# Kernel tuning notes

Hardware: AMD Instinct MI355X
Metric: run time of the kernel (lower is better)

## Reference

```python
import jax, jax.numpy as jnp
import numpy as np

B, L, HID = 2, 2048, 4096
NH, NKV, HD = 16, 4, 64
BLOCK = 16
THETA = 8000000.0
EPS = 1e-6
NEG = jnp.finfo(jnp.float32).min


def _rope_tables(theta, L, hd):
    inv_freq = 1.0 / (theta ** (np.arange(0, hd, 2, dtype=np.float32) / hd))  # [hd/2]
    t = np.arange(L, dtype=np.float32)
    freqs = np.outer(t, inv_freq)                      # [L, hd/2]
    emb = np.concatenate([freqs, freqs], axis=-1)      # [L, hd]
    return jnp.asarray(np.cos(emb)), jnp.asarray(np.sin(emb))


def setup_inputs() -> dict:
    key = jax.random.key(0)
    k1, k2, k3 = jax.random.split(key, 3)
    hidden_states = jax.random.normal(k1, (B, L, HID), dtype=jnp.float32)
    Wqkv = jax.random.normal(k2, (HID, (NH + 2 * NKV) * HD), dtype=jnp.float32) * 0.006
    Wo = jax.random.normal(k3, (NH * HD, HID), dtype=jnp.float32) * 0.006
    q_norm_w = jnp.ones((HD,), dtype=jnp.float32)
    k_norm_w = jnp.ones((HD,), dtype=jnp.float32)
    # block-diagonal causal additive mask [1,1,L,L]
    idx = jnp.arange(L)
    same_block = (idx[:, None] // BLOCK) == (idx[None, :] // BLOCK)
    causal = idx[:, None] >= idx[None, :]
    attention_mask = jnp.where(same_block & causal, 0.0, NEG)[None, None].astype(jnp.float32)
    cos1, sin1 = _rope_tables(THETA, L, HD)
    cos = jnp.broadcast_to(cos1[None], (B, L, HD))
    sin = jnp.broadcast_to(sin1[None], (B, L, HD))
    return {"hidden_states": hidden_states, "attention_mask": attention_mask,
            "cos": cos, "sin": sin, "Wqkv": Wqkv, "Wo": Wo,
            "q_norm_w": q_norm_w, "k_norm_w": k_norm_w}


def _rms_norm(x, w):
    xf = x.astype(jnp.float32)
    var = jnp.mean(xf * xf, axis=-1, keepdims=True)
    return (xf * jax.lax.rsqrt(var + EPS)).astype(x.dtype) * w


def _rotate_half(x):
    x1, x2 = jnp.split(x, 2, axis=-1)
    return jnp.concatenate([-x2, x1], axis=-1)


def reference(hidden_states, attention_mask, cos, sin, Wqkv, Wo, q_norm_w, k_norm_w):
    Bc, Lc, _ = hidden_states.shape
    qkv = hidden_states @ Wqkv                                # [B,L,(NH+2NKV)*HD]
    qkv = qkv.reshape(Bc, Lc, NH + 2 * NKV, HD)
    q, k, v = jnp.split(qkv, [NH, NH + NKV], axis=2)
    q = q.transpose(0, 2, 1, 3)                               # [B,NH,L,HD]
    k = k.transpose(0, 2, 1, 3)                               # [B,NKV,L,HD]
    v = v.transpose(0, 2, 1, 3)
    q = _rms_norm(q, q_norm_w)
    k = _rms_norm(k, k_norm_w)
    c = cos[:, None]                                          # [B,1,L,HD]
    s = sin[:, None]
    q = q * c + _rotate_half(q) * s
    k = k * c + _rotate_half(k) * s
    groups = NH // NKV
    k = jnp.repeat(k, groups, axis=1)                         # [B,NH,L,HD]
    v = jnp.repeat(v, groups, axis=1)
    scale = 1.0 / jnp.sqrt(jnp.float32(HD))
    scores = jnp.einsum('bhqd,bhkd->bhqk', q, k) * scale + attention_mask
    probs = jax.nn.softmax(scores, axis=-1)
    out = jnp.einsum('bhqk,bhkd->bhqd', probs, v)             # [B,NH,L,HD]
    out = out.transpose(0, 2, 1, 3).reshape(Bc, Lc, NH * HD)
    return out @ Wo
```

## Files before the change

kernel.cpp:

```cpp
#include <hip/hip_runtime.h>
#include <hip/hip_bf16.h>
#include <cstdint>

#define B_SZ   2
#define L_SEQ  2048
#define HID    4096
#define NH     16
#define NKV    4
#define HD     64
#define NQKV   (NH + 2*NKV)
#define QKV_N  (NQKV*HD)
#define O_N    (NH*HD)
#define M_ROWS (B_SZ*L_SEQ)
#define EPSV   1e-6f

typedef __bf16  bf16x8_t  __attribute__((ext_vector_type(8)));
typedef float   f32x4_t   __attribute__((ext_vector_type(4)));
typedef unsigned short ushort8_t __attribute__((ext_vector_type(8)));

__device__ __forceinline__ unsigned short f2b(float f) {
    union { float f; uint32_t u; } v; v.f = f;
    uint32_t r = v.u + 0x7FFFu + ((v.u >> 16) & 1u);
    return (unsigned short)(r >> 16);
}
__device__ __forceinline__ float b2f(unsigned short u) {
    union { uint32_t u; float f; } v; v.u = ((uint32_t)u) << 16;
    return v.f;
}

__device__ __forceinline__ void gload_lds16(const void* g, void* l) {
    __builtin_amdgcn_global_load_lds(
        (__attribute__((address_space(1))) void*)(g),
        (__attribute__((address_space(3))) void*)(l),
        16, 0, 0);
}

#define BARF() do { asm volatile("" ::: "memory"); \
                    __builtin_amdgcn_s_barrier();  \
                    asm volatile("" ::: "memory"); } while (0)

template <int N> __device__ __forceinline__ void vmcnt_wait() {
    if constexpr (N == 5)      asm volatile("s_waitcnt vmcnt(5)" ::: "memory");
    else if constexpr (N == 6) asm volatile("s_waitcnt vmcnt(6)" ::: "memory");
    else                       asm volatile("s_waitcnt vmcnt(0)" ::: "memory");
}

__global__ __launch_bounds__(256) void cvt_f32_bf16(const float* __restrict__ in,
                                                    unsigned short* __restrict__ out,
                                                    int n8) {
    int i = blockIdx.x * 256 + threadIdx.x;
    if (i >= n8) return;
    const float4* p = (const float4*)(in + (size_t)i * 8);
    float4 a = p[0], b = p[1];
    ushort8_t o;
    o[0]=f2b(a.x); o[1]=f2b(a.y); o[2]=f2b(a.z); o[3]=f2b(a.w);
    o[4]=f2b(b.x); o[5]=f2b(b.y); o[6]=f2b(b.z); o[7]=f2b(b.w);
    *(ushort8_t*)(out + (size_t)i * 8) = o;
}

__global__ __launch_bounds__(256) void transpose_f32_bf16(const float* __restrict__ in,
                                                          unsigned short* __restrict__ out,
                                                          int R, int C) {
    __shared__ float t[32][33];
    const int c0 = blockIdx.x * 32;
    const int r0 = blockIdx.y * 32;
    const int tx = threadIdx.x & 31;
    const int ty = threadIdx.x >> 5;
    #pragma unroll
    for (int i = 0; i < 32; i += 8)
        t[ty + i][tx] = in[(size_t)(r0 + ty + i) * C + c0 + tx];
    __syncthreads();
    #pragma unroll
    for (int i = 0; i < 32; i += 8)
        out[(size_t)(c0 + ty + i) * R + r0 + tx] = f2b(t[tx][ty + i]);
}

template <int BM, int BN, int NWM, int NWN, bool OBF16, typename OutT>
__global__ __launch_bounds__(512, 2)
void gemm_sb(const unsigned short* __restrict__ A,
             const unsigned short* __restrict__ Bt,
             OutT* __restrict__ C, int M, int N, int K) {
    constexpr int WM   = BM / NWM;
    constexpr int WN   = BN / NWN;
    constexpr int AF   = WM / 16;
    constexpr int BF   = WN / 16;
    constexpr int BUF  = (BM + BN) * 64;
    constexpr int AR   = BM / 64;
    constexpr int BR   = BN / 64;
    constexpr int RNDS = AR + BR;

    __shared__ unsigned short smem[3 * BUF];

    const int tid  = threadIdx.x;
    const int lane = tid & 63;
    const int wave = tid >> 6;
    const int wm   = wave / NWN;
    const int wn   = wave % NWN;
    const int fr   = lane & 15;
    const int fq   = lane >> 4;

    const int nbx = N / BN;
    int bid = blockIdx.x;
    const int cpx = gridDim.x >> 3;
    bid = (bid & 7) * cpx + (bid >> 3);
    const int bx = bid % nbx, by = bid / nbx;
    const int m0 = by * BM, n0 = bx * BN;

    const int srow = tid >> 3;
    const int scs  = ((tid & 7) ^ (srow & 7)) << 3;
    const unsigned short* gA = A  + (size_t)(m0 + srow) * K + scs;
    const unsigned short* gB = Bt + (size_t)(n0 + srow) * K + scs;

    const int cx0 = ((fq)     ^ (fr & 7)) << 3;
    const int cx1 = ((4 | fq) ^ (fr & 7)) << 3;

    f32x4_t acc[AF][BF];
    #pragma unroll
    for (int m = 0; m < AF; m++)
        #pragma unroll
        for (int n = 0; n < BF; n++)
            acc[m][n] = (f32x4_t){0.f, 0.f, 0.f, 0.f};

    const int NT = K >> 6;

#define STAGE_SB(T) { const int pb = ((T) % 3) * BUF; \
    _Pragma("unroll") for (int q = 0; q < AR; ++q) \
        gload_lds16(gA + (size_t)(q*64)*K + ((size_t)(T) << 6), \
                    &smem[pb + q*4096 + tid*8]); \
    _Pragma("unroll") for (int q = 0; q < BR; ++q) \
        gload_lds16(gB + (size_t)(q*64)*K + ((size_t)(T) << 6), \
                    &smem[pb + BM*64 + q*4096 + tid*8]); }

    STAGE_SB(0);
    STAGE_SB(1);
    vmcnt_wait<RNDS>();

    for (int t = 0; t < NT; ++t) {
        const int sb = (t % 3) * BUF;
        BARF();

        bf16x8_t a0[AF], b0[BF];
        #pragma unroll
        for (int mm = 0; mm < AF; ++mm)
            a0[mm] = *(const bf16x8_t*)&smem[sb + (wm*WM + mm*16 + fr)*64 + cx0];
        #pragma unroll
        for (int nn = 0; nn < BF; ++nn)
            b0[nn] = *(const bf16x8_t*)&smem[sb + BM*64 + (wn*WN + nn*16 + fr)*64 + cx0];

        if (t + 2 < NT) STAGE_SB(t + 2);

        __builtin_amdgcn_s_setprio(1);
        #pragma unroll
        for (int mm = 0; mm < AF; ++mm)
            #pragma unroll
            for (int nn = 0; nn < BF; ++nn)
                acc[mm][nn] = __builtin_amdgcn_mfma_f32_16x16x32_bf16(
                    a0[mm], b0[nn], acc[mm][nn], 0, 0, 0);
        __builtin_amdgcn_s_setprio(0);

        bf16x8_t a1[AF], b1[BF];
        #pragma unroll
        for (int mm = 0; mm < AF; ++mm)
            a1[mm] = *(const bf16x8_t*)&smem[sb + (wm*WM + mm*16 + fr)*64 + cx1];
        #pragma unroll
        for (int nn = 0; nn < BF; ++nn)
            b1[nn] = *(const bf16x8_t*)&smem[sb + BM*64 + (wn*WN + nn*16 + fr)*64 + cx1];

        __builtin_amdgcn_s_setprio(1);
        #pragma unroll
        for (int mm = 0; mm < AF; ++mm)
            #pragma unroll
            for (int nn = 0; nn < BF; ++nn)
                acc[mm][nn] = __builtin_amdgcn_mfma_f32_16x16x32_bf16(
                    a1[mm], b1[nn], acc[mm][nn], 0, 0, 0);
        __builtin_amdgcn_s_setprio(0);

        if (t + 2 < NT)      { vmcnt_wait<RNDS>(); }
        else if (t + 1 < NT) { vmcnt_wait<0>(); }
    }
#undef STAGE_SB

    const int crow = m0 + wm * WM + fq * 4;
    const int ccol = n0 + wn * WN + fr;
    #pragma unroll
    for (int m = 0; m < AF; m++)
        #pragma unroll
        for (int n = 0; n < BF; n++)
            #pragma unroll
            for (int rr = 0; rr < 4; rr++) {
                const size_t idx = (size_t)(crow + m*16 + rr) * N + ccol + n*16;
                if constexpr (OBF16) C[idx] = (OutT)f2b(acc[m][n][rr]);
                else                 C[idx] = (OutT)acc[m][n][rr];
            }
}

__global__ __launch_bounds__(64) void attn_fused(const unsigned short* __restrict__ qkv,
                                                 const float* __restrict__ cosb,
                                                 const float* __restrict__ sinb,
                                                 const float* __restrict__ qw,
                                                 const float* __restrict__ kw,
                                                 unsigned short* __restrict__ out) {
    const int h    = blockIdx.x & (NH - 1);
    const int blk  = (blockIdx.x >> 4) & 127;
    const int b    = blockIdx.x >> 11;
    const int pos0 = blk * 16;
    const int kvh  = h >> 2;

    const int lane = threadIdx.x;
    const int r    = lane >> 2;
    const int qp   = lane & 3;
    const int d0   = qp * 16;

    __shared__ float qs[16][65];
    __shared__ float ks[16][65];
    __shared__ float vs[16][65];
    __shared__ float ps[16][17];

    const size_t rowb = ((size_t)(b * L_SEQ + pos0 + r)) * NQKV;
    const unsigned short* qptr = qkv + (rowb + h) * HD + d0;
    const unsigned short* kptr = qkv + (rowb + NH + kvh) * HD + d0;
    const unsigned short* vptr = qkv + (rowb + NH + NKV + kvh) * HD + d0;
    const size_t csrow = ((size_t)(b * L_SEQ + pos0 + r)) * HD + d0;

    float q[16], k[16], v[16], cs[16], sn[16];
    {
        ushort8_t q0 = *(const ushort8_t*)&qptr[0], q1 = *(const ushort8_t*)&qptr[8];
        ushort8_t k0 = *(const ushort8_t*)&kptr[0], k1 = *(const ushort8_t*)&kptr[8];
        ushort8_t v0 = *(const ushort8_t*)&vptr[0], v1 = *(const ushort8_t*)&vptr[8];
        #pragma unroll
        for (int i = 0; i < 8; i++) {
            q[i] = b2f(q0[i]); q[i+8] = b2f(q1[i]);
            k[i] = b2f(k0[i]); k[i+8] = b2f(k1[i]);
            v[i] = b2f(v0[i]); v[i+8] = b2f(v1[i]);
        }
        #pragma unroll
        for (int i = 0; i < 16; i += 4) {
            *(float4*)&cs[i] = *(const float4*)&cosb[csrow + i];
            *(float4*)&sn[i] = *(const float4*)&sinb[csrow + i];
        }
    }

    float sq = 0.f, sk = 0.f;
    #pragma unroll
    for (int i = 0; i < 16; i++) { sq += q[i]*q[i]; sk += k[i]*k[i]; }
    sq += __shfl_xor(sq, 1); sq += __shfl_xor(sq, 2);
    sk += __shfl_xor(sk, 1); sk += __shfl_xor(sk, 2);
    const float rq = rsqrtf(sq * (1.f / HD) + EPSV);
    const float rk = rsqrtf(sk * (1.f / HD) + EPSV);

    const float sgn = (qp < 2) ? -1.f : 1.f;
    #pragma unroll
    for (int i = 0; i < 16; i++) {
        float qn = q[i] * rq * qw[d0 + i];
        float kn = k[i] * rk * kw[d0 + i];
        float qo = __shfl_xor(qn, 2);
        float ko = __shfl_xor(kn, 2);
        qs[r][d0 + i] = qn * cs[i] + sgn * qo * sn[i];
        ks[r][d0 + i] = kn * cs[i] + sgn * ko * sn[i];
        vs[r][d0 + i] = v[i];
    }
    __syncthreads();

    float sc[4] = {0.f, 0.f, 0.f, 0.f};
    for (int d = 0; d < 64; d++) {
        const float qd = qs[r][d];
        sc[0] += qd * ks[qp     ][d];
        sc[1] += qd * ks[qp +  4][d];
        sc[2] += qd * ks[qp +  8][d];
        sc[3] += qd * ks[qp + 12][d];
    }
    #pragma unroll
    for (int cc = 0; cc < 4; cc++) {
        const int c = qp + cc * 4;
        sc[cc] = (c <= r) ? sc[cc] * 0.125f : -3.0e38f;
    }
    float mx = fmaxf(fmaxf(sc[0], sc[1]), fmaxf(sc[2], sc[3]));
    mx = fmaxf(mx, __shfl_xor(mx, 1));
    mx = fmaxf(mx, __shfl_xor(mx, 2));
    float e[4], sum = 0.f;
    #pragma unroll
    for (int cc = 0; cc < 4; cc++) { e[cc] = __expf(sc[cc] - mx); sum += e[cc]; }
    sum += __shfl_xor(sum, 1); sum += __shfl_xor(sum, 2);
    const float inv = 1.f / sum;
    #pragma unroll
    for (int cc = 0; cc < 4; cc++) ps[r][qp + cc * 4] = e[cc] * inv;
    __syncthreads();

    float o[16];
    #pragma unroll
    for (int i = 0; i < 16; i++) o[i] = 0.f;
    #pragma unroll
    for (int c = 0; c < 16; c++) {
        const float p = ps[r][c];
        #pragma unroll
        for (int i = 0; i < 16; i++) o[i] += p * vs[c][d0 + i];
    }

    __attribute__((aligned(16))) unsigned short ob[16];
    #pragma unroll
    for (int i = 0; i < 16; i++) ob[i] = f2b(o[i]);
    unsigned short* optr = out + (((size_t)(b * L_SEQ + pos0 + r) * NH + h) * HD) + d0;
    *(uint4*)optr       = *(uint4*)&ob[0];
    *((uint4*)optr + 1) = *(uint4*)&ob[8];
}

extern "C" void kernel_launch(void* const* d_in, const int* in_sizes, int n_in,
                              void* d_out, int out_size, void* d_ws, size_t ws_size,
                              hipStream_t stream) {
    const float* hid  = (const float*)d_in[0];
    const float* cosb = (const float*)d_in[2];
    const float* sinb = (const float*)d_in[3];
    const float* Wqkv = (const float*)d_in[4];
    const float* Wo   = (const float*)d_in[5];
    const float* qw   = (const float*)d_in[6];
    const float* kw   = (const float*)d_in[7];
    float* outp = (float*)d_out;

    char* ws = (char*)d_ws;
    unsigned short* Hb    = (unsigned short*)ws; ws += (size_t)M_ROWS * HID * 2;
    unsigned short* WqkvT = (unsigned short*)ws; ws += (size_t)QKV_N * HID * 2;
    unsigned short* WoT   = (unsigned short*)ws; ws += (size_t)HID * O_N * 2;
    unsigned short* qkvb  = (unsigned short*)ws; ws += (size_t)M_ROWS * QKV_N * 2;
    unsigned short* attnb = (unsigned short*)ws;

    {
        int n8 = (M_ROWS * HID) / 8;
        cvt_f32_bf16<<<(n8 + 255) / 256, 256, 0, stream>>>(hid, Hb, n8);
    }
    transpose_f32_bf16<<<dim3(QKV_N / 32, HID / 32), 256, 0, stream>>>(Wqkv, WqkvT, HID, QKV_N);
    transpose_f32_bf16<<<dim3(HID / 32, O_N / 32),  256, 0, stream>>>(Wo,   WoT,   O_N, HID);

    gemm_sb<128, 192, 2, 4, true, unsigned short>
        <<<dim3((M_ROWS / 128) * (QKV_N / 192)), 512, 0, stream>>>
        (Hb, WqkvT, qkvb, M_ROWS, QKV_N, HID);

    attn_fused<<<dim3(B_SZ * (L_SEQ / 16) * NH), 64, 0, stream>>>(qkvb, cosb, sinb, qw, kw, attnb);

    gemm_sb<256, 128, 4, 2, false, float>
        <<<dim3((M_ROWS / 256) * (HID / 128)), 512, 0, stream>>>
        (attnb, WoT, outp, M_ROWS, HID, O_N);
}
```

Measured before the change: 151.4 us.

## Generalize GEMM over K-tile and pipeline depth; retile output projection GEMM

After: 143.9 us. 5.0% less time.

```diff
diff --git a/kernel.cpp b/kernel.cpp
--- a/kernel.cpp
+++ b/kernel.cpp
@@ -40,9 +40,13 @@
                     asm volatile("" ::: "memory"); } while (0)
 
 template <int N> __device__ __forceinline__ void vmcnt_wait() {
-    if constexpr (N == 5)      asm volatile("s_waitcnt vmcnt(5)" ::: "memory");
-    else if constexpr (N == 6) asm volatile("s_waitcnt vmcnt(6)" ::: "memory");
-    else                       asm volatile("s_waitcnt vmcnt(0)" ::: "memory");
+    if constexpr (N == 4)       asm volatile("s_waitcnt vmcnt(4)"  ::: "memory");
+    else if constexpr (N == 5)  asm volatile("s_waitcnt vmcnt(5)"  ::: "memory");
+    else if constexpr (N == 6)  asm volatile("s_waitcnt vmcnt(6)"  ::: "memory");
+    else if constexpr (N == 8)  asm volatile("s_waitcnt vmcnt(8)"  ::: "memory");
+    else if constexpr (N == 10) asm volatile("s_waitcnt vmcnt(10)" ::: "memory");
+    else if constexpr (N == 12) asm volatile("s_waitcnt vmcnt(12)" ::: "memory");
+    else                        asm volatile("s_waitcnt vmcnt(0)"  ::: "memory");
 }
 
 __global__ __launch_bounds__(256) void cvt_f32_bf16(const float* __restrict__ in,
@@ -75,21 +79,24 @@
         out[(size_t)(c0 + ty + i) * R + r0 + tx] = f2b(t[tx][ty + i]);
 }
 
-template <int BM, int BN, int NWM, int NWN, bool OBF16, typename OutT>
+template <int BM, int BN, int BK, int NBUF, int NWM, int NWN, bool OBF16, typename OutT>
 __global__ __launch_bounds__(512, 2)
 void gemm_sb(const unsigned short* __restrict__ A,
              const unsigned short* __restrict__ Bt,
              OutT* __restrict__ C, int M, int N, int K) {
-    constexpr int WM   = BM / NWM;
-    constexpr int WN   = BN / NWN;
-    constexpr int AF   = WM / 16;
-    constexpr int BF   = WN / 16;
-    constexpr int BUF  = (BM + BN) * 64;
-    constexpr int AR   = BM / 64;
-    constexpr int BR   = BN / 64;
-    constexpr int RNDS = AR + BR;
-
-    __shared__ unsigned short smem[3 * BUF];
+    constexpr int WM    = BM / NWM;
+    constexpr int WN    = BN / NWN;
+    constexpr int AF    = WM / 16;
+    constexpr int BF    = WN / 16;
+    constexpr int KK    = BK / 32;
+    constexpr int BUF   = (BM + BN) * BK;
+    constexpr int ROWS  = 4096 / BK;
+    constexpr int AR    = BM / ROWS;
+    constexpr int BR    = BN / ROWS;
+    constexpr int RNDS  = AR + BR;
+    constexpr int DEPTH = NBUF - 2;
+
+    __shared__ unsigned short smem[NBUF * BUF];
 
     const int tid  = threadIdx.x;
     const int lane = tid & 63;
@@ -106,13 +113,14 @@
     const int bx = bid % nbx, by = bid / nbx;
     const int m0 = by * BM, n0 = bx * BN;
 
-    const int srow = tid >> 3;
-    const int scs  = ((tid & 7) ^ (srow & 7)) << 3;
+    const int srow = tid / (BK / 8);
+    const int sch  = tid & (BK / 8 - 1);
+    const int ssw  = (BK == 64) ? (srow & 7) : ((srow >> 1) & 3);
+    const int scs  = (sch ^ ssw) << 3;
     const unsigned short* gA = A  + (size_t)(m0 + srow) * K + scs;
     const unsigned short* gB = Bt + (size_t)(n0 + srow) * K + scs;
 
-    const int cx0 = ((fq)     ^ (fr & 7)) << 3;
-    const int cx1 = ((4 | fq) ^ (fr & 7)) << 3;
+    const int frsw = (BK == 64) ? (fr & 7) : ((fr >> 1) & 3);
 
     f32x4_t acc[AF][BF];
     #pragma unroll
@@ -121,64 +129,60 @@
         for (int n = 0; n < BF; n++)
             acc[m][n] = (f32x4_t){0.f, 0.f, 0.f, 0.f};
 
-    const int NT = K >> 6;
-
-#define STAGE_SB(T) { const int pb = ((T) % 3) * BUF; \
-    _Pragma("unroll") for (int q = 0; q < AR; ++q) \
-        gload_lds16(gA + (size_t)(q*64)*K + ((size_t)(T) << 6), \
-                    &smem[pb + q*4096 + tid*8]); \
-    _Pragma("unroll") for (int q = 0; q < BR; ++q) \
-        gload_lds16(gB + (size_t)(q*64)*K + ((size_t)(T) << 6), \
-                    &smem[pb + BM*64 + q*4096 + tid*8]); }
-
-    STAGE_SB(0);
-    STAGE_SB(1);
-    vmcnt_wait<RNDS>();
+    const int NT = K / BK;
+
+    auto STAGE = [&](int T) {
+        const int pb = (T % NBUF) * BUF;
+        #pragma unroll
+        for (int q = 0; q < AR; ++q)
+            gload_lds16(gA + (size_t)(q * ROWS) * K + (size_t)T * BK,
+                        &smem[pb + q * 4096 + tid * 8]);
+        #pragma unroll
+        for (int q = 0; q < BR; ++q)
+            gload_lds16(gB + (size_t)(q * ROWS) * K + (size_t)T * BK,
+                        &smem[pb + BM * BK + q * 4096 + tid * 8]);
+    };
+
+    #pragma unroll
+    for (int pt = 0; pt < NBUF - 1; ++pt) STAGE(pt);
+    vmcnt_wait<DEPTH * RNDS>();
 
     for (int t = 0; t < NT; ++t) {
-        const int sb = (t % 3) * BUF;
+        const int sb = (t % NBUF) * BUF;
         BARF();
 
-        bf16x8_t a0[AF], b0[BF];
-        #pragma unroll
-        for (int mm = 0; mm < AF; ++mm)
-            a0[mm] = *(const bf16x8_t*)&smem[sb + (wm*WM + mm*16 + fr)*64 + cx0];
-        #pragma unroll
-        for (int nn = 0; nn < BF; ++nn)
-            b0[nn] = *(const bf16x8_t*)&smem[sb + BM*64 + (wn*WN + nn*16 + fr)*64 + cx0];
-
-        if (t + 2 < NT) STAGE_SB(t + 2);
-
-        __builtin_amdgcn_s_setprio(1);
-        #pragma unroll
-        for (int mm = 0; mm < AF; ++mm)
+        #pragma unroll
+        for (int kk = 0; kk < KK; ++kk) {
+            const int cxk = (((kk * 4 + fq) ^ frsw)) << 3;
+            bf16x8_t aF[AF], bF[BF];
+            #pragma unroll
+            for (int mm = 0; mm < AF; ++mm)
+                aF[mm] = *(const bf16x8_t*)&smem[sb + (wm*WM + mm*16 + fr)*BK + cxk];
             #pragma unroll
             for (int nn = 0; nn < BF; ++nn)
-                acc[mm][nn] = __builtin_amdgcn_mfma_f32_16x16x32_bf16(
-                    a0[mm], b0[nn], acc[mm][nn], 0, 0, 0);
-        __builtin_amdgcn_s_setprio(0);
-
-        bf16x8_t a1[AF], b1[BF];
-        #pragma unroll
-        for (int mm = 0; mm < AF; ++mm)
-            a1[mm] = *(const bf16x8_t*)&smem[sb + (wm*WM + mm*16 + fr)*64 + cx1];
-        #pragma unroll
-        for (int nn = 0; nn < BF; ++nn)
-            b1[nn] = *(const bf16x8_t*)&smem[sb + BM*64 + (wn*WN + nn*16 + fr)*64 + cx1];
-
-        __builtin_amdgcn_s_setprio(1);
-        #pragma unroll
-        for (int mm = 0; mm < AF; ++mm)
+                bF[nn] = *(const bf16x8_t*)&smem[sb + BM*BK + (wn*WN + nn*16 + fr)*BK + cxk];
+
+            if (kk == 0 && t + NBUF - 1 < NT) STAGE(t + NBUF - 1);
+
+            __builtin_amdgcn_s_setprio(1);
             #pragma unroll
-            for (int nn = 0; nn < BF; ++nn)
-                acc[mm][nn] = __builtin_amdgcn_mfma_f32_16x16x32_bf16(
-                    a1[mm], b1[nn], acc[mm][nn], 0, 0, 0);
-        __builtin_amdgcn_s_setprio(0);
-
-        if (t + 2 < NT)      { vmcnt_wait<RNDS>(); }
-        else if (t + 1 < NT) { vmcnt_wait<0>(); }
-    }
-#undef STAGE_SB
+            for (int mm = 0; mm < AF; ++mm)
+                #pragma unroll
+                for (int nn = 0; nn < BF; ++nn)
+                    acc[mm][nn] = __builtin_amdgcn_mfma_f32_16x16x32_bf16(
+                        aF[mm], bF[nn], acc[mm][nn], 0, 0, 0);
+            __builtin_amdgcn_s_setprio(0);
+        }
+
+        if constexpr (DEPTH == 2) {
+            if (t + 3 < NT)      { vmcnt_wait<2 * RNDS>(); }
+            else if (t + 2 < NT) { vmcnt_wait<RNDS>(); }
+            else if (t + 1 < NT) { vmcnt_wait<0>(); }
+        } else {
+            if (t + 2 < NT)      { vmcnt_wait<RNDS>(); }
+            else if (t + 1 < NT) { vmcnt_wait<0>(); }
+        }
+    }
 
     const int crow = m0 + wm * WM + fq * 4;
     const int ccol = n0 + wn * WN + fr;
@@ -330,13 +334,13 @@
     transpose_f32_bf16<<<dim3(QKV_N / 32, HID / 32), 256, 0, stream>>>(Wqkv, WqkvT, HID, QKV_N);
     transpose_f32_bf16<<<dim3(HID / 32, O_N / 32),  256, 0, stream>>>(Wo,   WoT,   O_N, HID);
 
-    gemm_sb<128, 192, 2, 4, true, unsigned short>
+    gemm_sb<128, 192, 64, 3, 2, 4, true, unsigned short>
         <<<dim3((M_ROWS / 128) * (QKV_N / 192)), 512, 0, stream>>>
         (Hb, WqkvT, qkvb, M_ROWS, QKV_N, HID);
 
     attn_fused<<<dim3(B_SZ * (L_SEQ / 16) * NH), 64, 0, stream>>>(qkvb, cosb, sinb, qw, kw, attnb);
 
-    gemm_sb<256, 128, 4, 2, false, float>
-        <<<dim3((M_ROWS / 256) * (HID / 128)), 512, 0, stream>>>
+    gemm_sb<256, 256, 32, 4, 2, 4, false, float>
+        <<<dim3((M_ROWS / 256) * (HID / 256)), 512, 0, stream>>>
         (attnb, WoT, outp, M_ROWS, HID, O_N);
 }
```
